# Optimization experiments

Measured on AMD Instinct MI355X. Metric: run time of the kernel, lower is better.

## Reference

```python
import jax, jax.numpy as jnp
import numpy as np
import math

CAPACITY_FACTOR = 1.0

def setup_inputs() -> dict:
    key = jax.random.key(0)
    k1, k2 = jax.random.split(key)
    x = jax.random.normal(k1, (8192, 2048), dtype=jnp.float32)
    wg = jax.random.normal(k2, (64, 2048), dtype=jnp.float32) * (1.0 / np.sqrt(2048))
    return {"x": x, "wg": wg}

def reference(x, wg):
    # logits = Linear(model_dim, num_experts, bias=False)(x)
    logits = jnp.einsum('sd,ed->se', x, wg)
    gates = jax.nn.softmax(logits, axis=1)  # [s, e]
    s, e = gates.shape
    capacity = math.ceil(s / e * CAPACITY_FACTOR)  # static
    indices1_s = jnp.argmax(gates, axis=1)  # [s]
    mask1 = jax.nn.one_hot(indices1_s, e, dtype=jnp.int32)  # [s, e]
    locations1 = jnp.cumsum(mask1, axis=0) - 1  # position within each expert queue
    # aux load-balancing loss
    me = jnp.mean(gates, axis=0)
    ce = jnp.mean(mask1.astype(gates.dtype), axis=0)
    l_aux = jnp.mean(me * ce) * (e * e)
    # drop tokens over capacity
    mask1 = mask1 * (locations1 < capacity).astype(jnp.int32)
    locations1_s = jnp.sum(locations1 * mask1, axis=1)  # [s] int
    mask1_float = mask1.astype(gates.dtype)
    gates1_s = jnp.sum(gates * mask1_float, axis=1)  # 'se,se->s'
    gates1 = gates1_s[:, None] * mask1_float         # 's,se->se'
    locations1_sc = jax.nn.one_hot(locations1_s, capacity, dtype=gates.dtype)  # [s, c]
    combine_weights = gates1[:, :, None] * locations1_sc[:, None, :]  # 'se,sc->sec'
    dispatch_mask = combine_weights.astype(bool)
    return l_aux, combine_weights, dispatch_mask
```

## Files before the change

kernel.cpp:

```cpp
#include <hip/hip_runtime.h>
#include <cstdint>
#include <cstddef>


#define S_TOK 8192
#define NEXP 64
#define DIM 2048
#define CAP 128
#define COMB_ELEMS ((size_t)S_TOK * NEXP * CAP)
#define OUT_ELEMS (1 + 2 * COMB_ELEMS)

#define TOK_TILE 128
#define NSLICE 4
#define KSLICE (DIM / NSLICE)
#define KC 32

__global__ __launch_bounds__(256) void logits_kernel(
    const float* __restrict__ x, const float* __restrict__ wg,
    float* __restrict__ P)
{
    __shared__ float xs[KC][132];
    __shared__ float wsh[KC][68];

    const int tid  = threadIdx.x;
    const int tile  = blockIdx.x >> 2;
    const int slice = blockIdx.x & 3;
    const int tok0 = tile * TOK_TILE;
    const int k0   = slice * KSLICE;

    const int tt = tid >> 4;
    const int te = tid & 15;

    float acc[8][4];
#pragma unroll
    for (int i = 0; i < 8; ++i)
#pragma unroll
        for (int j = 0; j < 4; ++j) acc[i][j] = 0.0f;

    const int we  = tid & 63;
    const int wkq = tid >> 6;

    float4 xv[4], wv[2];
#pragma unroll
    for (int r = 0; r < 4; ++r) {
        int idx = tid + 256 * r;
        int t = idx >> 3, kq = idx & 7;
        xv[r] = *(const float4*)(x + (size_t)(tok0 + t) * DIM + k0 + 4 * kq);
    }
    wv[0] = *(const float4*)(wg + (size_t)we * DIM + k0 + 4 * wkq);
    wv[1] = *(const float4*)(wg + (size_t)we * DIM + k0 + 4 * (wkq + 4));

    for (int kc = 0; kc < KSLICE; kc += KC) {
        __syncthreads();
#pragma unroll
        for (int r = 0; r < 4; ++r) {
            int idx = tid + 256 * r;
            int t = idx >> 3, k4 = (idx & 7) * 4;
            xs[k4 + 0][t] = xv[r].x; xs[k4 + 1][t] = xv[r].y;
            xs[k4 + 2][t] = xv[r].z; xs[k4 + 3][t] = xv[r].w;
        }
        {
            int k4 = 4 * wkq;
            wsh[k4 + 0][we] = wv[0].x; wsh[k4 + 1][we] = wv[0].y;
            wsh[k4 + 2][we] = wv[0].z; wsh[k4 + 3][we] = wv[0].w;
            int k4b = k4 + 16;
            wsh[k4b + 0][we] = wv[1].x; wsh[k4b + 1][we] = wv[1].y;
            wsh[k4b + 2][we] = wv[1].z; wsh[k4b + 3][we] = wv[1].w;
        }
        __syncthreads();
        if (kc + KC < KSLICE) {
#pragma unroll
            for (int r = 0; r < 4; ++r) {
                int idx = tid + 256 * r;
                int t = idx >> 3, kq = idx & 7;
                xv[r] = *(const float4*)(x + (size_t)(tok0 + t) * DIM + k0 + kc + KC + 4 * kq);
            }
            wv[0] = *(const float4*)(wg + (size_t)we * DIM + k0 + kc + KC + 4 * wkq);
            wv[1] = *(const float4*)(wg + (size_t)we * DIM + k0 + kc + KC + 4 * (wkq + 4));
        }
#pragma unroll 8
        for (int k = 0; k < KC; ++k) {
            float4 a0 = *(const float4*)&xs[k][8 * tt];
            float4 a1 = *(const float4*)&xs[k][8 * tt + 4];
            float4 b  = *(const float4*)&wsh[k][4 * te];
            const float* ap0 = &a0.x; const float* ap1 = &a1.x; const float* bp = &b.x;
#pragma unroll
            for (int i = 0; i < 4; ++i)
#pragma unroll
                for (int j = 0; j < 4; ++j) {
                    acc[i][j]     += ap0[i] * bp[j];
                    acc[i + 4][j] += ap1[i] * bp[j];
                }
        }
    }

#pragma unroll
    for (int i = 0; i < 8; ++i) {
        size_t off = ((size_t)slice * S_TOK + tok0 + 8 * tt + i) * NEXP + 4 * te;
        float4 v = { acc[i][0], acc[i][1], acc[i][2], acc[i][3] };
        *(float4*)(P + off) = v;
    }
}

__global__ __launch_bounds__(256) void reduce_kernel(
    const float* __restrict__ P,
    int* __restrict__ idx_out, float* __restrict__ gate_out,
    float* __restrict__ gsum)
{
    __shared__ float sme[NEXP];
    const int tid = threadIdx.x;
    const int tok0 = blockIdx.x * 32;
    const int ty = tid >> 5;
    const int tx = tid & 31;
    const int t0 = ty * 4;
    const int e0 = tx * 2;

    if (tid < NEXP) sme[tid] = 0.0f;

    float gm0 = 0.0f, gm1 = 0.0f;
#pragma unroll
    for (int i = 0; i < 4; ++i) {
        int tok = tok0 + t0 + i;
        float l0 = 0.0f, l1 = 0.0f;
#pragma unroll
        for (int s = 0; s < NSLICE; ++s) {
            float2 p = *(const float2*)&P[((size_t)s * S_TOK + tok) * NEXP + e0];
            l0 += p.x; l1 += p.y;
        }
        float v; int ix;
        if (l1 > l0) { v = l1; ix = e0 + 1; } else { v = l0; ix = e0; }
#pragma unroll
        for (int off = 16; off; off >>= 1) {
            float ov = __shfl_xor(v, off, 32);
            int   oi = __shfl_xor(ix, off, 32);
            if (ov > v || (ov == v && oi < ix)) { v = ov; ix = oi; }
        }
        float z0 = __expf(l0 - v), z1 = __expf(l1 - v);
        float zs = z0 + z1;
#pragma unroll
        for (int off = 16; off; off >>= 1) zs += __shfl_xor(zs, off, 32);
        float inv = 1.0f / zs;
        gm0 += z0 * inv; gm1 += z1 * inv;
        if (tx == 0) {
            idx_out[tok]  = ix;
            gate_out[tok] = inv;
        }
    }
    atomicAdd(&sme[e0], gm0);
    atomicAdd(&sme[e0 + 1], gm1);
    __syncthreads();
    if (tid < NEXP) atomicAdd(&gsum[tid], sme[tid]);
}

__global__ __launch_bounds__(1024) void scan_kernel(
    const int* __restrict__ idx, const float* __restrict__ gsum,
    int* __restrict__ loc_out, float* __restrict__ laux_out)
{
    __shared__ int wavecnt[16][NEXP];
    __shared__ int basecnt[NEXP];
    const int tid  = threadIdx.x;
    const int lane = tid & 63;
    const int wv   = tid >> 6;

    if (tid < NEXP) basecnt[tid] = 0;
    __syncthreads();

    for (int it = 0; it < S_TOK / 1024; ++it) {
        int tok = it * 1024 + tid;
        int e = idx[tok];
        unsigned long long m = ~0ull, lm = ~0ull;
#pragma unroll
        for (int b = 0; b < 6; ++b) {
            unsigned long long bal = __ballot((e >> b) & 1);
            m  &= ((e >> b) & 1)    ? bal : ~bal;
            lm &= ((lane >> b) & 1) ? bal : ~bal;
        }
        int rank = __popcll(m & ((1ull << lane) - 1ull));
        wavecnt[wv][lane] = __popcll(lm);
        __syncthreads();
        int off = 0;
        for (int w = 0; w < wv; ++w) off += wavecnt[w][e];
        loc_out[tok] = basecnt[e] + off + rank;
        __syncthreads();
        if (tid < NEXP) {
            int tot = 0;
#pragma unroll
            for (int w = 0; w < 16; ++w) tot += wavecnt[w][tid];
            basecnt[tid] += tot;
        }
        __syncthreads();
    }

    if (tid < NEXP) {
        float p = gsum[tid] * (float)basecnt[tid];
#pragma unroll
        for (int off = 32; off; off >>= 1) p += __shfl_xor(p, off, 64);
        if (tid == 0) laux_out[0] = p * 9.5367431640625e-07f;
    }
}

__global__ __launch_bounds__(256) void writer_kernel(
    const int* __restrict__ idx, const float* __restrict__ gate,
    const int* __restrict__ loc, const float* __restrict__ laux,
    float* __restrict__ out)
{
    size_t base = (size_t)blockIdx.x * 1024 + threadIdx.x;
#pragma unroll
    for (int r = 0; r < 4; ++r) {
        size_t j = base + 256 * (size_t)r;
        size_t i0 = j * 4;
        float4 v = { 0.0f, 0.0f, 0.0f, 0.0f };
        float* vp = &v.x;
#pragma unroll
        for (int jj = 0; jj < 4; ++jj) {
            size_t i = i0 + jj;
            if (i == 0) { vp[jj] = laux[0]; continue; }
            size_t q = i - 1;
            bool sel = q >= COMB_ELEMS;
            size_t p = sel ? q - COMB_ELEMS : q;
            int t = (int)(p >> 13);
            int rr = (int)(p & 8191);
            int e = rr >> 7, c = rr & 127;
            if (e == idx[t] && c == loc[t])
                vp[jj] = sel ? 1.0f : gate[t];
        }
        *(float4*)(out + i0) = v;
    }
    if (blockIdx.x == 0 && threadIdx.x == 0) {
        out[OUT_ELEMS - 1] = (idx[S_TOK - 1] == 63 && loc[S_TOK - 1] == 127) ? 1.0f : 0.0f;
    }
}

extern "C" void kernel_launch(void* const* d_in, const int* in_sizes, int n_in,
                              void* d_out, int out_size, void* d_ws, size_t ws_size,
                              hipStream_t stream) {
    const float* x  = (const float*)d_in[0];
    const float* wg = (const float*)d_in[1];
    float* out = (float*)d_out;

    int*   idx  = (int*)d_ws;
    float* gate = (float*)((char*)d_ws + 32768);
    float* gsum = (float*)((char*)d_ws + 65536);
    float* laux = (float*)((char*)d_ws + 65792);
    int*   loc  = (int*)((char*)d_ws + 66560);
    float* P    = (float*)((char*)d_ws + 131072);

    hipMemsetAsync(gsum, 0, NEXP * sizeof(float), stream);

    logits_kernel<<<(S_TOK / TOK_TILE) * NSLICE, 256, 0, stream>>>(x, wg, P);
    reduce_kernel<<<S_TOK / 32, 256, 0, stream>>>(P, idx, gate, gsum);
    scan_kernel<<<1, 1024, 0, stream>>>(idx, gsum, loc, laux);
    writer_kernel<<<32768, 256, 0, stream>>>(idx, gate, loc, laux, out);
}
```

Measured before the change: 619.7 us.

## Precompute flat token positions in scan and simplify dense output writer

The scan kernel now emits a flat (expert*CAP+loc) position and value per token for both the combine and dispatch halves, with -1 marking dropped tokens. The writer then needs one lookup per float4 instead of four index/loc/gate lookups with 64-bit index math, and each thread handles eight float4 stores. The gsum memset is folded into the logits kernel to save a launch. This relies on the writer being bound by output bandwidth, which is a large fraction of the runtime.

```diff
diff --git a/kernel.cpp b/kernel.cpp
--- a/kernel.cpp
+++ b/kernel.cpp
@@ -17,7 +17,7 @@
 
 __global__ __launch_bounds__(256) void logits_kernel(
     const float* __restrict__ x, const float* __restrict__ wg,
-    float* __restrict__ P)
+    float* __restrict__ P, float* __restrict__ gsum)
 {
     __shared__ float xs[KC][132];
     __shared__ float wsh[KC][68];
@@ -27,6 +27,8 @@
     const int slice = blockIdx.x & 3;
     const int tok0 = tile * TOK_TILE;
     const int k0   = slice * KSLICE;
+
+    if (blockIdx.x == 0 && tid < NEXP) gsum[tid] = 0.0f;
 
     const int tt = tid >> 4;
     const int te = tid & 15;
@@ -153,8 +155,10 @@
 }
 
 __global__ __launch_bounds__(1024) void scan_kernel(
-    const int* __restrict__ idx, const float* __restrict__ gsum,
-    int* __restrict__ loc_out, float* __restrict__ laux_out)
+    const int* __restrict__ idx, const float* __restrict__ gate,
+    const float* __restrict__ gsum,
+    int* __restrict__ pos2, float* __restrict__ val2,
+    float* __restrict__ laux_out)
 {
     __shared__ int wavecnt[16][NEXP];
     __shared__ int basecnt[NEXP];
@@ -180,7 +184,12 @@
         __syncthreads();
         int off = 0;
         for (int w = 0; w < wv; ++w) off += wavecnt[w][e];
-        loc_out[tok] = basecnt[e] + off + rank;
+        int loc = basecnt[e] + off + rank;
+        int p = (loc < CAP) ? (e * CAP + loc) : -1;
+        pos2[tok]         = p;
+        pos2[tok + S_TOK] = p;
+        val2[tok]         = gate[tok];
+        val2[tok + S_TOK] = 1.0f;
         __syncthreads();
         if (tid < NEXP) {
             int tot = 0;
@@ -200,34 +209,47 @@
 }
 
 __global__ __launch_bounds__(256) void writer_kernel(
-    const int* __restrict__ idx, const float* __restrict__ gate,
-    const int* __restrict__ loc, const float* __restrict__ laux,
-    float* __restrict__ out)
-{
-    size_t base = (size_t)blockIdx.x * 1024 + threadIdx.x;
-#pragma unroll
-    for (int r = 0; r < 4; ++r) {
-        size_t j = base + 256 * (size_t)r;
-        size_t i0 = j * 4;
+    const int* __restrict__ pos2, const float* __restrict__ val2,
+    const float* __restrict__ laux, float* __restrict__ out)
+{
+    const int tid = threadIdx.x;
+    size_t m0 = (size_t)blockIdx.x * 2048 + tid;
+#pragma unroll
+    for (int r = 0; r < 8; ++r) {
+        size_t m = m0 + 256 * (size_t)r;
         float4 v = { 0.0f, 0.0f, 0.0f, 0.0f };
-        float* vp = &v.x;
-#pragma unroll
-        for (int jj = 0; jj < 4; ++jj) {
-            size_t i = i0 + jj;
-            if (i == 0) { vp[jj] = laux[0]; continue; }
-            size_t q = i - 1;
-            bool sel = q >= COMB_ELEMS;
-            size_t p = sel ? q - COMB_ELEMS : q;
-            int t = (int)(p >> 13);
-            int rr = (int)(p & 8191);
-            int e = rr >> 7, c = rr & 127;
-            if (e == idx[t] && c == loc[t])
-                vp[jj] = sel ? 1.0f : gate[t];
-        }
-        *(float4*)(out + i0) = v;
-    }
-    if (blockIdx.x == 0 && threadIdx.x == 0) {
-        out[OUT_ELEMS - 1] = (idx[S_TOK - 1] == 63 && loc[S_TOK - 1] == 127) ? 1.0f : 0.0f;
+        if (m == 0) {
+            v.x = laux[0];
+            int p = pos2[0];
+            float val = val2[0];
+            v.y = (p == 0) ? val : 0.0f;
+            v.z = (p == 1) ? val : 0.0f;
+            v.w = (p == 2) ? val : 0.0f;
+        } else {
+            size_t q0 = 4 * m - 1;
+            int vt = (int)(q0 >> 13);
+            int w  = (int)(q0 & 8191);
+            int p  = pos2[vt];
+            float val = val2[vt];
+            if (w == 8191) {
+                v.x = (p == 8191) ? val : 0.0f;
+                int p2 = pos2[vt + 1];
+                float val2b = val2[vt + 1];
+                v.y = (p2 == 0) ? val2b : 0.0f;
+                v.z = (p2 == 1) ? val2b : 0.0f;
+                v.w = (p2 == 2) ? val2b : 0.0f;
+            } else {
+                unsigned d = (unsigned)(p - w);
+                v.x = (d == 0u) ? val : 0.0f;
+                v.y = (d == 1u) ? val : 0.0f;
+                v.z = (d == 2u) ? val : 0.0f;
+                v.w = (d == 3u) ? val : 0.0f;
+            }
+        }
+        *(float4*)(out + 4 * m) = v;
+    }
+    if (blockIdx.x == 0 && tid == 0) {
+        out[OUT_ELEMS - 1] = (pos2[2 * S_TOK - 1] == 8191) ? 1.0f : 0.0f;
     }
 }
 
@@ -242,13 +264,12 @@
     float* gate = (float*)((char*)d_ws + 32768);
     float* gsum = (float*)((char*)d_ws + 65536);
     float* laux = (float*)((char*)d_ws + 65792);
-    int*   loc  = (int*)((char*)d_ws + 66560);
-    float* P    = (float*)((char*)d_ws + 131072);
-
-    hipMemsetAsync(gsum, 0, NEXP * sizeof(float), stream);
-
-    logits_kernel<<<(S_TOK / TOK_TILE) * NSLICE, 256, 0, stream>>>(x, wg, P);
+    int*   pos2 = (int*)((char*)d_ws + 131072);
+    float* val2 = (float*)((char*)d_ws + 196608);
+    float* P    = (float*)((char*)d_ws + 262144);
+
+    logits_kernel<<<(S_TOK / TOK_TILE) * NSLICE, 256, 0, stream>>>(x, wg, P, gsum);
     reduce_kernel<<<S_TOK / 32, 256, 0, stream>>>(P, idx, gate, gsum);
-    scan_kernel<<<1, 1024, 0, stream>>>(idx, gsum, loc, laux);
-    writer_kernel<<<32768, 256, 0, stream>>>(idx, gate, loc, laux, out);
-}
+    scan_kernel<<<1, 1024, 0, stream>>>(idx, gate, gsum, pos2, val2, laux);
+    writer_kernel<<<16384, 256, 0, stream>>>(pos2, val2, laux, out);
+}
```

Measured after the change: 623.3 us. Within noise of the previous version (+0.6%).

## Zero output inside GEMM launch and scatter nonzeros from scan kernel

Applied to the files above, without the earlier changes.

Drops the dense writer kernel that checked every one of the ~134M output elements against per-token idx/loc. The output is now zero-filled by extra blocks appended to the logits GEMM launch, so the fill runs alongside the GEMM. The single-block scan then scatters the 2 nonzeros per kept token and writes l_aux directly. The gsum memset is folded into GEMM block 0. The zero-fill and the GEMM now compete for bandwidth and CUs within one launch, and correctness depends on stream ordering between the zero-fill and the later scatter.

```diff
diff --git a/kernel.cpp b/kernel.cpp
--- a/kernel.cpp
+++ b/kernel.cpp
@@ -9,24 +9,46 @@
 #define CAP 128
 #define COMB_ELEMS ((size_t)S_TOK * NEXP * CAP)
 #define OUT_ELEMS (1 + 2 * COMB_ELEMS)
+#define NQUAD (OUT_ELEMS / 4)
 
 #define TOK_TILE 128
 #define NSLICE 4
 #define KSLICE (DIM / NSLICE)
 #define KC 32
 
-__global__ __launch_bounds__(256) void logits_kernel(
+#define GEMM_BLKS 256
+#define ZERO_BLKS 768
+#define TOTAL_BLKS (GEMM_BLKS + ZERO_BLKS)
+#define QCHUNK 43691
+
+__global__ __launch_bounds__(256, 4) void fused_zero_gemm(
     const float* __restrict__ x, const float* __restrict__ wg,
-    float* __restrict__ P)
+    float* __restrict__ P, float* __restrict__ gsum,
+    float* __restrict__ out)
 {
+    const int tid = threadIdx.x;
+
+    if (blockIdx.x >= GEMM_BLKS) {
+        const int zb = blockIdx.x - GEMM_BLKS;
+        size_t begin = (size_t)zb * QCHUNK;
+        size_t end   = begin + QCHUNK;
+        if (end > (size_t)NQUAD) end = (size_t)NQUAD;
+        const float4 z = { 0.0f, 0.0f, 0.0f, 0.0f };
+        for (size_t q = begin + tid; q < end; q += 256)
+            *(float4*)(out + 4 * q) = z;
+        if (zb == 0 && tid == 0) out[OUT_ELEMS - 1] = 0.0f;
+        return;
+    }
+
     __shared__ float xs[KC][132];
     __shared__ float wsh[KC][68];
 
-    const int tid  = threadIdx.x;
     const int tile  = blockIdx.x >> 2;
     const int slice = blockIdx.x & 3;
     const int tok0 = tile * TOK_TILE;
     const int k0   = slice * KSLICE;
+
+    if (blockIdx.x == 0 && tid < NEXP) gsum[tid] = 0.0f;
 
     const int tt = tid >> 4;
     const int te = tid & 15;
@@ -152,9 +174,9 @@
     if (tid < NEXP) atomicAdd(&gsum[tid], sme[tid]);
 }
 
-__global__ __launch_bounds__(1024) void scan_kernel(
-    const int* __restrict__ idx, const float* __restrict__ gsum,
-    int* __restrict__ loc_out, float* __restrict__ laux_out)
+__global__ __launch_bounds__(1024) void scan_scatter(
+    const int* __restrict__ idx, const float* __restrict__ gate,
+    const float* __restrict__ gsum, float* __restrict__ out)
 {
     __shared__ int wavecnt[16][NEXP];
     __shared__ int basecnt[NEXP];
@@ -180,7 +202,12 @@
         __syncthreads();
         int off = 0;
         for (int w = 0; w < wv; ++w) off += wavecnt[w][e];
-        loc_out[tok] = basecnt[e] + off + rank;
+        int loc = basecnt[e] + off + rank;
+        if (loc < CAP) {
+            size_t base = 1 + (size_t)tok * (NEXP * CAP) + (size_t)e * CAP + loc;
+            out[base] = gate[tok];
+            out[base + COMB_ELEMS] = 1.0f;
+        }
         __syncthreads();
         if (tid < NEXP) {
             int tot = 0;
@@ -195,39 +222,7 @@
         float p = gsum[tid] * (float)basecnt[tid];
 #pragma unroll
         for (int off = 32; off; off >>= 1) p += __shfl_xor(p, off, 64);
-        if (tid == 0) laux_out[0] = p * 9.5367431640625e-07f;
-    }
-}
-
-__global__ __launch_bounds__(256) void writer_kernel(
-    const int* __restrict__ idx, const float* __restrict__ gate,
-    const int* __restrict__ loc, const float* __restrict__ laux,
-    float* __restrict__ out)
-{
-    size_t base = (size_t)blockIdx.x * 1024 + threadIdx.x;
-#pragma unroll
-    for (int r = 0; r < 4; ++r) {
-        size_t j = base + 256 * (size_t)r;
-        size_t i0 = j * 4;
-        float4 v = { 0.0f, 0.0f, 0.0f, 0.0f };
-        float* vp = &v.x;
-#pragma unroll
-        for (int jj = 0; jj < 4; ++jj) {
-            size_t i = i0 + jj;
-            if (i == 0) { vp[jj] = laux[0]; continue; }
-            size_t q = i - 1;
-            bool sel = q >= COMB_ELEMS;
-            size_t p = sel ? q - COMB_ELEMS : q;
-            int t = (int)(p >> 13);
-            int rr = (int)(p & 8191);
-            int e = rr >> 7, c = rr & 127;
-            if (e == idx[t] && c == loc[t])
-                vp[jj] = sel ? 1.0f : gate[t];
-        }
-        *(float4*)(out + i0) = v;
-    }
-    if (blockIdx.x == 0 && threadIdx.x == 0) {
-        out[OUT_ELEMS - 1] = (idx[S_TOK - 1] == 63 && loc[S_TOK - 1] == 127) ? 1.0f : 0.0f;
+        if (tid == 0) out[0] = p * 9.5367431640625e-07f;
     }
 }
 
@@ -241,14 +236,9 @@
     int*   idx  = (int*)d_ws;
     float* gate = (float*)((char*)d_ws + 32768);
     float* gsum = (float*)((char*)d_ws + 65536);
-    float* laux = (float*)((char*)d_ws + 65792);
-    int*   loc  = (int*)((char*)d_ws + 66560);
-    float* P    = (float*)((char*)d_ws + 131072);
-
-    hipMemsetAsync(gsum, 0, NEXP * sizeof(float), stream);
-
-    logits_kernel<<<(S_TOK / TOK_TILE) * NSLICE, 256, 0, stream>>>(x, wg, P);
+    float* P    = (float*)((char*)d_ws + 262144);
+
+    fused_zero_gemm<<<TOTAL_BLKS, 256, 0, stream>>>(x, wg, P, gsum, out);
     reduce_kernel<<<S_TOK / 32, 256, 0, stream>>>(P, idx, gate, gsum);
-    scan_kernel<<<1, 1024, 0, stream>>>(idx, gsum, loc, laux);
-    writer_kernel<<<32768, 256, 0, stream>>>(idx, gate, loc, laux, out);
-}
+    scan_scatter<<<1, 1024, 0, stream>>>(idx, gate, gsum, out);
+}
```

Result: no change. 615.6 us (-0.7%).
